# Performance work log

Measured on AMD Instinct MI355X. Metric: run time of the kernel, lower is better.

Reference implementation:

```python
import jax, jax.numpy as jnp
import numpy as np

NUM_HEADS = 16
NUM_KV_HEADS = 4
HEAD_SIZE = 128
SCALE = 1.0 / np.sqrt(128.0).astype(np.float32)
NEG_INF = -1e30


def setup_inputs() -> dict:
    key = jax.random.key(0)
    kq, kk, kv = jax.random.split(key, 3)
    B, S = 2, 2048
    query = jax.random.normal(kq, (B, NUM_HEADS, S, HEAD_SIZE), dtype=jnp.float32)
    k = jax.random.normal(kk, (B, NUM_KV_HEADS, S, HEAD_SIZE), dtype=jnp.float32)
    v = jax.random.normal(kv, (B, NUM_KV_HEADS, S, HEAD_SIZE), dtype=jnp.float32)
    return {"query": query, "key": k, "value": v}


def _attn(query, key, value):
    # query: [B, H, S, D]; key/value: [B, Hkv, S, D]; GQA with group = H // Hkv
    B, H, S, D = query.shape
    Hkv = key.shape[1]
    G = H // Hkv
    q = query.reshape(B, Hkv, G, S, D)
    # scores: [B, Hkv, G, Sq, Sk]
    scores = jnp.einsum('bkgsd,bktd->bkgst', q, key) * jnp.float32(SCALE)
    causal = jnp.tril(jnp.ones((S, S), dtype=bool))  # [Sq, Sk]
    scores = jnp.where(causal, scores, jnp.float32(NEG_INF))
    probs = jax.nn.softmax(scores, axis=-1)
    out = jnp.einsum('bkgst,bktd->bkgsd', probs, value)  # [B, Hkv, G, S, D]
    out = out.reshape(B, H, S, D)
    # transpose(1,2).reshape -> [B, S, H*D]
    return out.transpose(0, 2, 1, 3).reshape(B, S, H * D)


def reference(query, key, value):
    return _attn(query, key, value)
```

## Files before the change

kernel.cpp:

```cpp
#include <hip/hip_runtime.h>


#define S_LEN 2048
#define DH    128
#define NH    16
#define NKVH  4
#define NB    2
#define TQ    128
#define TK    64
#define NQT   (S_LEN / TQ)
#define QSCALE 0.12752749610559243f

typedef __attribute__((ext_vector_type(8))) short short8;
typedef __attribute__((ext_vector_type(4))) float f32x4;

#if __has_builtin(__builtin_amdgcn_exp2f)
#define EX2(x) __builtin_amdgcn_exp2f(x)
#else
#define EX2(x) exp2f(x)
#endif

__device__ __forceinline__ unsigned short bf1(float a) {
    union { float f; unsigned u; } x; x.f = a;
    return (unsigned short)((x.u + 0x8000u) >> 16);
}
__device__ __forceinline__ unsigned pk2(float a, float b) {
    union { float f; unsigned u; } x, y; x.f = a; y.f = b;
    return ((x.u + 0x8000u) >> 16) | ((y.u + 0x8000u) & 0xffff0000u);
}
__device__ __forceinline__ void cp16(const void* g, void* lds) {
    __builtin_amdgcn_global_load_lds(
        (const __attribute__((address_space(1))) void*)g,
        (__attribute__((address_space(3))) void*)lds, 16, 0, 0);
}

__global__ __launch_bounds__(256, 4)
void prepack(const float* __restrict__ K, const float* __restrict__ V,
             unsigned short* __restrict__ Kb, unsigned short* __restrict__ Vt) {
    if (blockIdx.y == 0) {
        const long long flat = (long long)blockIdx.x * 2048 + threadIdx.x * 8;
        const int s = (int)(flat >> 7) & (S_LEN - 1);
        const int d0 = (int)flat & 127;
        const float* p = K + flat;
        float4 x = *(const float4*)p;
        float4 y = *(const float4*)(p + 4);
        const int cs = (d0 >> 3) ^ (s & 7);
        uint4 o;
        o.x = pk2(x.x, x.y); o.y = pk2(x.z, x.w);
        o.z = pk2(y.x, y.y); o.w = pk2(y.z, y.w);
        *(uint4*)(Kb + (flat & ~127LL) + cs * 8) = o;
    } else {
        const int x = blockIdx.x;
        const int bkvh = x >> 7, sblk = (x >> 2) & 31, q = x & 3;
        const int tid = threadIdx.x;
        __shared__ unsigned Lt[64][17];
        const float* base = V + (size_t)bkvh * S_LEN * DH + (size_t)sblk * 64 * DH + q * 32;
#pragma unroll
        for (int j = 0; j < 2; ++j) {
            const int e = tid + j * 256;
            const int s = e >> 3, c4 = e & 7;
            float4 v = *(const float4*)(base + (size_t)s * DH + c4 * 4);
            Lt[s][c4 * 2]     = pk2(v.x, v.y);
            Lt[s][c4 * 2 + 1] = pk2(v.z, v.w);
        }
        __syncthreads();
        const unsigned short* lt = (const unsigned short*)&Lt[0][0];
        const int d_loc = tid >> 3, pc = tid & 7;
        const int d = q * 32 + d_loc;
        const int c_log = pc ^ (d & 7);
        unsigned short vv[8];
#pragma unroll
        for (int j = 0; j < 8; ++j) {
            const int kp = c_log * 8 + j;
            const int kv = (kp & 3) * 16 + (kp >> 2);
            vv[j] = lt[kv * 34 + d_loc];
        }
        uint4 o;
        o.x = (unsigned)vv[0] | ((unsigned)vv[1] << 16);
        o.y = (unsigned)vv[2] | ((unsigned)vv[3] << 16);
        o.z = (unsigned)vv[4] | ((unsigned)vv[5] << 16);
        o.w = (unsigned)vv[6] | ((unsigned)vv[7] << 16);
        *(uint4*)(Vt + (size_t)bkvh * S_LEN * DH + (size_t)d * S_LEN + sblk * 64 + pc * 8) = o;
    }
}

__global__ __launch_bounds__(256, 2)
void attn_fwd(const float* __restrict__ Q,
              const unsigned short* __restrict__ Kb,
              const unsigned short* __restrict__ Vtg,
              float* __restrict__ O) {
    const int n  = blockIdx.x;
    const int x  = n & 15;
    const int h  = (n >> 4) & 15;
    const int b  = n >> 8;
    const int qt = b ? x : (NQT - 1 - x);
    const int kvh = h >> 2;

    const int tid  = threadIdx.x;
    const int w    = tid >> 6;
    const int lane = tid & 63;
    const int quad = lane >> 4;
    const int l16  = lane & 15;
    const int swz  = l16 & 7;

    __shared__ alignas(16) unsigned short Kl[2][TK][DH];
    __shared__ alignas(16) unsigned short Vl[DH][TK];
    __shared__ alignas(16) unsigned short Pl[TQ][TK];

    const unsigned short* kb = Kb  + ((size_t)b * NKVH + kvh) * (size_t)(S_LEN * DH);
    const unsigned short* vb = Vtg + ((size_t)b * NKVH + kvh) * (size_t)(S_LEN * DH);

    const int wq0 = qt * TQ + w * 32;
    short8 aq[2][4];
#pragma unroll
    for (int sub = 0; sub < 2; ++sub) {
        const float* qp = Q + (((size_t)b * NH + h) * S_LEN + wq0 + sub * 16 + l16) * DH;
#pragma unroll
        for (int dc = 0; dc < 4; ++dc) {
            float4 xx = *(const float4*)(qp + dc * 32 + quad * 8);
            float4 yy = *(const float4*)(qp + dc * 32 + quad * 8 + 4);
            union { unsigned u[4]; short8 s; } t;
            t.u[0] = pk2(xx.x * QSCALE, xx.y * QSCALE);
            t.u[1] = pk2(xx.z * QSCALE, xx.w * QSCALE);
            t.u[2] = pk2(yy.x * QSCALE, yy.y * QSCALE);
            t.u[3] = pk2(yy.z * QSCALE, yy.w * QSCALE);
            aq[sub][dc] = t.s;
        }
    }

    f32x4 o[2][8];
#pragma unroll
    for (int sub = 0; sub < 2; ++sub)
#pragma unroll
        for (int ch = 0; ch < 8; ++ch) o[sub][ch] = (f32x4){0.f, 0.f, 0.f, 0.f};
    float lsum[2][4];
#pragma unroll
    for (int sub = 0; sub < 2; ++sub)
#pragma unroll
        for (int r = 0; r < 4; ++r) lsum[sub][r] = 0.f;

    const int nt  = 2 * qt + 2;
    const int ntw = 2 * qt + 1 + (w >> 1);

#pragma unroll
    for (int i = 0; i < 4; ++i)
        cp16((const char*)kb + w * 4096 + i * 1024 + lane * 16,
             (char*)&Kl[0][0][0] + w * 4096 + i * 1024);
    __syncthreads();

    for (int t = 0; t < nt; ++t) {
        const int j0 = t * TK;
#pragma unroll
        for (int i = 0; i < 4; ++i) {
            const int row  = w * 32 + i * 8 + (lane >> 3);
            const int colB = (lane & 7) * 16;
            cp16((const char*)vb + (size_t)row * (S_LEN * 2) + j0 * 2 + colB,
                 (char*)&Vl[0][0] + w * 4096 + i * 1024);
        }
        if (t + 1 < nt) {
            const char* ks = (const char*)(kb + (size_t)(j0 + TK) * DH);
            char* kd = (char*)&Kl[(t + 1) & 1][0][0];
#pragma unroll
            for (int i = 0; i < 4; ++i)
                cp16(ks + w * 4096 + i * 1024 + lane * 16, kd + w * 4096 + i * 1024);
        }

        const unsigned short (*Kc)[DH] = Kl[t & 1];
        const bool active = (t < ntw);
        const bool diag = (t == ntw - 1);
        f32x4 s[2][4];

        if (active) {
#pragma unroll
            for (int sub = 0; sub < 2; ++sub)
#pragma unroll
                for (int k4 = 0; k4 < 4; ++k4) s[sub][k4] = (f32x4){0.f, 0.f, 0.f, 0.f};
#pragma unroll
            for (int dc = 0; dc < 4; ++dc) {
#pragma unroll
                for (int k4 = 0; k4 < 4; ++k4) {
                    short8 bk = *(const short8*)&Kc[k4 * 16 + l16][((dc * 4 + quad) ^ swz) * 8];
                    s[0][k4] = __builtin_amdgcn_mfma_f32_16x16x32_bf16(aq[0][dc], bk, s[0][k4], 0, 0, 0);
                    s[1][k4] = __builtin_amdgcn_mfma_f32_16x16x32_bf16(aq[1][dc], bk, s[1][k4], 0, 0, 0);
                }
            }
#pragma unroll
            for (int sub = 0; sub < 2; ++sub) {
                const int rb = wq0 + sub * 16 + quad * 4;
#pragma unroll
                for (int r = 0; r < 4; ++r) {
                    float v0 = s[sub][0][r], v1 = s[sub][1][r];
                    float v2 = s[sub][2][r], v3 = s[sub][3][r];
                    if (diag) {
                        const int row = rb + r;
                        if (j0 + l16      > row) v0 = -1e30f;
                        if (j0 + 16 + l16 > row) v1 = -1e30f;
                        if (j0 + 32 + l16 > row) v2 = -1e30f;
                        if (j0 + 48 + l16 > row) v3 = -1e30f;
                    }
                    float p0 = EX2(v0), p1 = EX2(v1), p2 = EX2(v2), p3 = EX2(v3);
                    lsum[sub][r] += (p0 + p1) + (p2 + p3);
                    const int prow = w * 32 + sub * 16 + quad * 4 + r;
                    const int chs = (l16 >> 1) ^ (prow & 7);
                    *(uint2*)&Pl[prow][chs * 8 + (l16 & 1) * 4] =
                        make_uint2(pk2(p0, p1), pk2(p2, p3));
                }
            }
        }

        __syncthreads();

        if (active) {
#pragma unroll
            for (int kc = 0; kc < 2; ++kc) {
                const int pr0 = w * 32 + l16;
                short8 ap0 = *(const short8*)&Pl[pr0][(((kc * 4 + quad) ^ swz)) * 8];
                short8 ap1 = *(const short8*)&Pl[pr0 + 16][(((kc * 4 + quad) ^ swz)) * 8];
#pragma unroll
                for (int ch = 0; ch < 8; ++ch) {
                    short8 bv = *(const short8*)&Vl[ch * 16 + l16][((kc * 4 + quad) ^ swz) * 8];
                    o[0][ch] = __builtin_amdgcn_mfma_f32_16x16x32_bf16(ap0, bv, o[0][ch], 0, 0, 0);
                    o[1][ch] = __builtin_amdgcn_mfma_f32_16x16x32_bf16(ap1, bv, o[1][ch], 0, 0, 0);
                }
            }
        }

        __syncthreads();
    }

#pragma unroll
    for (int sub = 0; sub < 2; ++sub) {
#pragma unroll
        for (int r = 0; r < 4; ++r) {
            float rs = lsum[sub][r];
            rs += __shfl_xor(rs, 1);
            rs += __shfl_xor(rs, 2);
            rs += __shfl_xor(rs, 4);
            rs += __shfl_xor(rs, 8);
            const float invl = 1.f / rs;
            const int row = wq0 + sub * 16 + quad * 4 + r;
            float* op = O + ((size_t)b * S_LEN + row) * (NH * DH) + h * DH;
#pragma unroll
            for (int ch = 0; ch < 8; ++ch)
                op[ch * 16 + l16] = o[sub][ch][r] * invl;
        }
    }
}

extern "C" void kernel_launch(void* const* d_in, const int* in_sizes, int n_in,
                              void* d_out, int out_size, void* d_ws, size_t ws_size,
                              hipStream_t stream) {
    const float* Q = (const float*)d_in[0];
    const float* K = (const float*)d_in[1];
    const float* V = (const float*)d_in[2];
    float* O = (float*)d_out;
    unsigned short* Kb = (unsigned short*)d_ws;
    unsigned short* Vt = Kb + (size_t)NB * NKVH * S_LEN * DH;
    dim3 pgrid(NB * NKVH * (S_LEN / 16), 2);
    prepack<<<pgrid, 256, 0, stream>>>(K, V, Kb, Vt);
    attn_fwd<<<dim3(512), 256, 0, stream>>>(Q, Kb, Vt, O);
}
```

Baseline: 158.6 us.

## Split long causal query tiles across blocks and add partial-sum combine kernel

```diff
diff --git a/kernel.cpp b/kernel.cpp
--- a/kernel.cpp
+++ b/kernel.cpp
@@ -10,6 +10,7 @@
 #define TK    64
 #define NQT   (S_LEN / TQ)
 #define QSCALE 0.12752749610559243f
+#define NSPLIT 11
 
 typedef __attribute__((ext_vector_type(8))) short short8;
 typedef __attribute__((ext_vector_type(4))) float f32x4;
@@ -20,9 +21,19 @@
 #define EX2(x) exp2f(x)
 #endif
 
+__constant__ signed char SLOT_QT[16][2] = {
+    {15,-1},{15,-1},{14,-1},{14,-1},{13, 0},{13,-1},{12, 2},{12, 1},
+    {11, 5},{11, 5},{10, 6},{10, 6},{ 9, 7},{ 9, 7},{ 4, 3},{ 8, 8}};
+__constant__ signed char SLOT_MODE[16][2] = {
+    { 0,-1},{ 1,-1},{ 0,-1},{ 1,-1},{ 0, 2},{ 1,-1},{ 0, 2},{ 1, 2},
+    { 0, 0},{ 1, 1},{ 0, 0},{ 1, 1},{ 0, 0},{ 1, 1},{ 2, 2},{ 0, 1}};
+
 __device__ __forceinline__ unsigned short bf1(float a) {
     union { float f; unsigned u; } x; x.f = a;
     return (unsigned short)((x.u + 0x8000u) >> 16);
+}
+__device__ __forceinline__ float bf2f(unsigned short a) {
+    union { float f; unsigned u; } x; x.u = (unsigned)a << 16; return x.f;
 }
 __device__ __forceinline__ unsigned pk2(float a, float b) {
     union { float f; unsigned u; } x, y; x.f = a; y.f = b;
@@ -88,13 +99,18 @@
 void attn_fwd(const float* __restrict__ Q,
               const unsigned short* __restrict__ Kb,
               const unsigned short* __restrict__ Vtg,
-              float* __restrict__ O) {
-    const int n  = blockIdx.x;
-    const int x  = n & 15;
-    const int h  = (n >> 4) & 15;
-    const int b  = n >> 8;
-    const int qt = b ? x : (NQT - 1 - x);
-    const int kvh = h >> 2;
+              float* __restrict__ O,
+              unsigned short* __restrict__ OP,
+              float* __restrict__ LP) {
+    const int n   = blockIdx.x;
+    const int xcd = n & 7;
+    const int b   = xcd >> 2;
+    const int kvh = xcd & 3;
+    const int j   = n >> 3;
+    const int hl  = j >> 4;
+    const int slot = j & 15;
+    const int h   = kvh * 4 + hl;
+    const int hh  = xcd * 4 + hl;
 
     const int tid  = threadIdx.x;
     const int w    = tid >> 6;
@@ -107,143 +123,205 @@
     __shared__ alignas(16) unsigned short Vl[DH][TK];
     __shared__ alignas(16) unsigned short Pl[TQ][TK];
 
-    const unsigned short* kb = Kb  + ((size_t)b * NKVH + kvh) * (size_t)(S_LEN * DH);
-    const unsigned short* vb = Vtg + ((size_t)b * NKVH + kvh) * (size_t)(S_LEN * DH);
-
-    const int wq0 = qt * TQ + w * 32;
-    short8 aq[2][4];
-#pragma unroll
-    for (int sub = 0; sub < 2; ++sub) {
-        const float* qp = Q + (((size_t)b * NH + h) * S_LEN + wq0 + sub * 16 + l16) * DH;
-#pragma unroll
-        for (int dc = 0; dc < 4; ++dc) {
-            float4 xx = *(const float4*)(qp + dc * 32 + quad * 8);
-            float4 yy = *(const float4*)(qp + dc * 32 + quad * 8 + 4);
-            union { unsigned u[4]; short8 s; } t;
-            t.u[0] = pk2(xx.x * QSCALE, xx.y * QSCALE);
-            t.u[1] = pk2(xx.z * QSCALE, xx.w * QSCALE);
-            t.u[2] = pk2(yy.x * QSCALE, yy.y * QSCALE);
-            t.u[3] = pk2(yy.z * QSCALE, yy.w * QSCALE);
-            aq[sub][dc] = t.s;
-        }
-    }
-
-    f32x4 o[2][8];
-#pragma unroll
-    for (int sub = 0; sub < 2; ++sub)
-#pragma unroll
-        for (int ch = 0; ch < 8; ++ch) o[sub][ch] = (f32x4){0.f, 0.f, 0.f, 0.f};
-    float lsum[2][4];
-#pragma unroll
-    for (int sub = 0; sub < 2; ++sub)
-#pragma unroll
-        for (int r = 0; r < 4; ++r) lsum[sub][r] = 0.f;
-
-    const int nt  = 2 * qt + 2;
-    const int ntw = 2 * qt + 1 + (w >> 1);
-
-#pragma unroll
-    for (int i = 0; i < 4; ++i)
-        cp16((const char*)kb + w * 4096 + i * 1024 + lane * 16,
-             (char*)&Kl[0][0][0] + w * 4096 + i * 1024);
-    __syncthreads();
-
-    for (int t = 0; t < nt; ++t) {
-        const int j0 = t * TK;
-#pragma unroll
-        for (int i = 0; i < 4; ++i) {
-            const int row  = w * 32 + i * 8 + (lane >> 3);
-            const int colB = (lane & 7) * 16;
-            cp16((const char*)vb + (size_t)row * (S_LEN * 2) + j0 * 2 + colB,
-                 (char*)&Vl[0][0] + w * 4096 + i * 1024);
-        }
-        if (t + 1 < nt) {
-            const char* ks = (const char*)(kb + (size_t)(j0 + TK) * DH);
-            char* kd = (char*)&Kl[(t + 1) & 1][0][0];
-#pragma unroll
-            for (int i = 0; i < 4; ++i)
-                cp16(ks + w * 4096 + i * 1024 + lane * 16, kd + w * 4096 + i * 1024);
-        }
-
-        const unsigned short (*Kc)[DH] = Kl[t & 1];
-        const bool active = (t < ntw);
-        const bool diag = (t == ntw - 1);
-        f32x4 s[2][4];
-
-        if (active) {
-#pragma unroll
-            for (int sub = 0; sub < 2; ++sub)
-#pragma unroll
-                for (int k4 = 0; k4 < 4; ++k4) s[sub][k4] = (f32x4){0.f, 0.f, 0.f, 0.f};
+    const unsigned short* kb = Kb  + (size_t)xcd * (S_LEN * DH);
+    const unsigned short* vb = Vtg + (size_t)xcd * (S_LEN * DH);
+
+    for (int it = 0; it < 2; ++it) {
+        const int qt   = SLOT_QT[slot][it];
+        const int mode = SLOT_MODE[slot][it];
+        if (mode < 0) continue;
+        const int nt   = 2 * qt + 2;
+        const int t_lo = (mode == 1) ? (qt + 1) : 0;
+        const int t_hi = (mode == 0) ? (qt + 1) : nt;
+        const int Tw   = 2 * qt + 1 + (w >> 1);
+
+        const int wq0 = qt * TQ + w * 32;
+        short8 aq[2][4];
+#pragma unroll
+        for (int sub = 0; sub < 2; ++sub) {
+            const float* qp = Q + (((size_t)b * NH + h) * S_LEN + wq0 + sub * 16 + l16) * DH;
 #pragma unroll
             for (int dc = 0; dc < 4; ++dc) {
-#pragma unroll
-                for (int k4 = 0; k4 < 4; ++k4) {
-                    short8 bk = *(const short8*)&Kc[k4 * 16 + l16][((dc * 4 + quad) ^ swz) * 8];
-                    s[0][k4] = __builtin_amdgcn_mfma_f32_16x16x32_bf16(aq[0][dc], bk, s[0][k4], 0, 0, 0);
-                    s[1][k4] = __builtin_amdgcn_mfma_f32_16x16x32_bf16(aq[1][dc], bk, s[1][k4], 0, 0, 0);
-                }
-            }
+                float4 xx = *(const float4*)(qp + dc * 32 + quad * 8);
+                float4 yy = *(const float4*)(qp + dc * 32 + quad * 8 + 4);
+                union { unsigned u[4]; short8 s; } tt;
+                tt.u[0] = pk2(xx.x * QSCALE, xx.y * QSCALE);
+                tt.u[1] = pk2(xx.z * QSCALE, xx.w * QSCALE);
+                tt.u[2] = pk2(yy.x * QSCALE, yy.y * QSCALE);
+                tt.u[3] = pk2(yy.z * QSCALE, yy.w * QSCALE);
+                aq[sub][dc] = tt.s;
+            }
+        }
+
+        f32x4 o[2][8];
+#pragma unroll
+        for (int sub = 0; sub < 2; ++sub)
+#pragma unroll
+            for (int ch = 0; ch < 8; ++ch) o[sub][ch] = (f32x4){0.f, 0.f, 0.f, 0.f};
+        float lsum[2][4];
+#pragma unroll
+        for (int sub = 0; sub < 2; ++sub)
+#pragma unroll
+            for (int r = 0; r < 4; ++r) lsum[sub][r] = 0.f;
+
+#pragma unroll
+        for (int i = 0; i < 4; ++i)
+            cp16((const char*)(kb + (size_t)t_lo * TK * DH) + w * 4096 + i * 1024 + lane * 16,
+                 (char*)&Kl[t_lo & 1][0][0] + w * 4096 + i * 1024);
+        __syncthreads();
+
+        for (int t = t_lo; t < t_hi; ++t) {
+            const int j0 = t * TK;
+#pragma unroll
+            for (int i = 0; i < 4; ++i) {
+                const int row  = w * 32 + i * 8 + (lane >> 3);
+                const int colB = (lane & 7) * 16;
+                cp16((const char*)vb + (size_t)row * (S_LEN * 2) + j0 * 2 + colB,
+                     (char*)&Vl[0][0] + w * 4096 + i * 1024);
+            }
+            if (t + 1 < t_hi) {
+                const char* ks = (const char*)(kb + (size_t)(j0 + TK) * DH);
+                char* kd = (char*)&Kl[(t + 1) & 1][0][0];
+#pragma unroll
+                for (int i = 0; i < 4; ++i)
+                    cp16(ks + w * 4096 + i * 1024 + lane * 16, kd + w * 4096 + i * 1024);
+            }
+
+            const unsigned short (*Kc)[DH] = Kl[t & 1];
+            const bool active = (t < Tw);
+            const bool diag = (t == Tw - 1);
+            f32x4 s[2][4];
+
+            if (active) {
+#pragma unroll
+                for (int sub = 0; sub < 2; ++sub)
+#pragma unroll
+                    for (int k4 = 0; k4 < 4; ++k4) s[sub][k4] = (f32x4){0.f, 0.f, 0.f, 0.f};
+#pragma unroll
+                for (int dc = 0; dc < 4; ++dc) {
+#pragma unroll
+                    for (int k4 = 0; k4 < 4; ++k4) {
+                        short8 bk = *(const short8*)&Kc[k4 * 16 + l16][((dc * 4 + quad) ^ swz) * 8];
+                        s[0][k4] = __builtin_amdgcn_mfma_f32_16x16x32_bf16(aq[0][dc], bk, s[0][k4], 0, 0, 0);
+                        s[1][k4] = __builtin_amdgcn_mfma_f32_16x16x32_bf16(aq[1][dc], bk, s[1][k4], 0, 0, 0);
+                    }
+                }
+#pragma unroll
+                for (int sub = 0; sub < 2; ++sub) {
+                    const int rb = wq0 + sub * 16 + quad * 4;
+#pragma unroll
+                    for (int r = 0; r < 4; ++r) {
+                        float v0 = s[sub][0][r], v1 = s[sub][1][r];
+                        float v2 = s[sub][2][r], v3 = s[sub][3][r];
+                        if (diag) {
+                            const int row = rb + r;
+                            if (j0 + l16      > row) v0 = -1e30f;
+                            if (j0 + 16 + l16 > row) v1 = -1e30f;
+                            if (j0 + 32 + l16 > row) v2 = -1e30f;
+                            if (j0 + 48 + l16 > row) v3 = -1e30f;
+                        }
+                        float p0 = EX2(v0), p1 = EX2(v1), p2 = EX2(v2), p3 = EX2(v3);
+                        lsum[sub][r] += (p0 + p1) + (p2 + p3);
+                        const int prow = w * 32 + sub * 16 + quad * 4 + r;
+                        const int chs = (l16 >> 1) ^ (prow & 7);
+                        *(uint2*)&Pl[prow][chs * 8 + (l16 & 1) * 4] =
+                            make_uint2(pk2(p0, p1), pk2(p2, p3));
+                    }
+                }
+            }
+
+            __syncthreads();
+
+            if (active) {
+#pragma unroll
+                for (int kc = 0; kc < 2; ++kc) {
+                    const int pr0 = w * 32 + l16;
+                    short8 ap0 = *(const short8*)&Pl[pr0][(((kc * 4 + quad) ^ swz)) * 8];
+                    short8 ap1 = *(const short8*)&Pl[pr0 + 16][(((kc * 4 + quad) ^ swz)) * 8];
+#pragma unroll
+                    for (int ch = 0; ch < 8; ++ch) {
+                        short8 bv = *(const short8*)&Vl[ch * 16 + l16][((kc * 4 + quad) ^ swz) * 8];
+                        o[0][ch] = __builtin_amdgcn_mfma_f32_16x16x32_bf16(ap0, bv, o[0][ch], 0, 0, 0);
+                        o[1][ch] = __builtin_amdgcn_mfma_f32_16x16x32_bf16(ap1, bv, o[1][ch], 0, 0, 0);
+                    }
+                }
+            }
+
+            __syncthreads();
+        }
+
+        if (mode == 2) {
 #pragma unroll
             for (int sub = 0; sub < 2; ++sub) {
-                const int rb = wq0 + sub * 16 + quad * 4;
 #pragma unroll
                 for (int r = 0; r < 4; ++r) {
-                    float v0 = s[sub][0][r], v1 = s[sub][1][r];
-                    float v2 = s[sub][2][r], v3 = s[sub][3][r];
-                    if (diag) {
-                        const int row = rb + r;
-                        if (j0 + l16      > row) v0 = -1e30f;
-                        if (j0 + 16 + l16 > row) v1 = -1e30f;
-                        if (j0 + 32 + l16 > row) v2 = -1e30f;
-                        if (j0 + 48 + l16 > row) v3 = -1e30f;
-                    }
-                    float p0 = EX2(v0), p1 = EX2(v1), p2 = EX2(v2), p3 = EX2(v3);
-                    lsum[sub][r] += (p0 + p1) + (p2 + p3);
-                    const int prow = w * 32 + sub * 16 + quad * 4 + r;
-                    const int chs = (l16 >> 1) ^ (prow & 7);
-                    *(uint2*)&Pl[prow][chs * 8 + (l16 & 1) * 4] =
-                        make_uint2(pk2(p0, p1), pk2(p2, p3));
-                }
-            }
-        }
-
-        __syncthreads();
-
-        if (active) {
-#pragma unroll
-            for (int kc = 0; kc < 2; ++kc) {
-                const int pr0 = w * 32 + l16;
-                short8 ap0 = *(const short8*)&Pl[pr0][(((kc * 4 + quad) ^ swz)) * 8];
-                short8 ap1 = *(const short8*)&Pl[pr0 + 16][(((kc * 4 + quad) ^ swz)) * 8];
-#pragma unroll
-                for (int ch = 0; ch < 8; ++ch) {
-                    short8 bv = *(const short8*)&Vl[ch * 16 + l16][((kc * 4 + quad) ^ swz) * 8];
-                    o[0][ch] = __builtin_amdgcn_mfma_f32_16x16x32_bf16(ap0, bv, o[0][ch], 0, 0, 0);
-                    o[1][ch] = __builtin_amdgcn_mfma_f32_16x16x32_bf16(ap1, bv, o[1][ch], 0, 0, 0);
-                }
-            }
-        }
-
+                    float rs = lsum[sub][r];
+                    rs += __shfl_xor(rs, 1);
+                    rs += __shfl_xor(rs, 2);
+                    rs += __shfl_xor(rs, 4);
+                    rs += __shfl_xor(rs, 8);
+                    const float invl = 1.f / rs;
+                    const int row = wq0 + sub * 16 + quad * 4 + r;
+                    float* op = O + ((size_t)b * S_LEN + row) * (NH * DH) + h * DH;
+#pragma unroll
+                    for (int ch = 0; ch < 8; ++ch)
+                        op[ch * 16 + l16] = o[sub][ch][r] * invl;
+                }
+            }
+        } else {
+            const size_t pbase = ((size_t)(hh * NSPLIT + (qt - 5)) * 2 + mode) * (128 * 128);
+            unsigned short* opp = OP + pbase;
+            float* lpp = LP + ((size_t)(hh * NSPLIT + (qt - 5)) * 2 + mode) * 128;
+#pragma unroll
+            for (int sub = 0; sub < 2; ++sub) {
+#pragma unroll
+                for (int r = 0; r < 4; ++r) {
+                    float rs = lsum[sub][r];
+                    rs += __shfl_xor(rs, 1);
+                    rs += __shfl_xor(rs, 2);
+                    rs += __shfl_xor(rs, 4);
+                    rs += __shfl_xor(rs, 8);
+                    const int lrow = w * 32 + sub * 16 + quad * 4 + r;
+                    if (l16 == 0) lpp[lrow] = rs;
+#pragma unroll
+                    for (int ch = 0; ch < 8; ++ch)
+                        opp[(size_t)lrow * 128 + ch * 16 + l16] = bf1(o[sub][ch][r]);
+                }
+            }
+        }
         __syncthreads();
     }
-
-#pragma unroll
-    for (int sub = 0; sub < 2; ++sub) {
-#pragma unroll
-        for (int r = 0; r < 4; ++r) {
-            float rs = lsum[sub][r];
-            rs += __shfl_xor(rs, 1);
-            rs += __shfl_xor(rs, 2);
-            rs += __shfl_xor(rs, 4);
-            rs += __shfl_xor(rs, 8);
-            const float invl = 1.f / rs;
-            const int row = wq0 + sub * 16 + quad * 4 + r;
-            float* op = O + ((size_t)b * S_LEN + row) * (NH * DH) + h * DH;
-#pragma unroll
-            for (int ch = 0; ch < 8; ++ch)
-                op[ch * 16 + l16] = o[sub][ch][r] * invl;
-        }
+}
+
+__global__ __launch_bounds__(256, 4)
+void combine(const unsigned short* __restrict__ OP, const float* __restrict__ LP,
+             float* __restrict__ O) {
+    const int cb = blockIdx.x;
+    const int hh = cb / NSPLIT, qi = cb - hh * NSPLIT;
+    const int qt = qi + 5;
+    const int b = hh >> 4, kvh = (hh >> 2) & 3, hl = hh & 3, h = kvh * 4 + hl;
+    __shared__ float Linv[128];
+    if (threadIdx.x < 128) {
+        const size_t lb = (size_t)(hh * NSPLIT + qi) * 2 * 128;
+        Linv[threadIdx.x] = 1.f / (LP[lb + threadIdx.x] + LP[lb + 128 + threadIdx.x]);
+    }
+    __syncthreads();
+    const unsigned short* pa = OP + (size_t)(hh * NSPLIT + qi) * 2 * 16384;
+    const unsigned short* pb = pa + 16384;
+    float* ob = O + ((size_t)b * S_LEN + qt * 128) * (NH * DH) + h * DH;
+#pragma unroll
+    for (int i = 0; i < 16; ++i) {
+        const int flat = i * 1024 + threadIdx.x * 4;
+        const int row = flat >> 7, d = flat & 127;
+        ushort4 a = *(const ushort4*)(pa + flat);
+        ushort4 bq = *(const ushort4*)(pb + flat);
+        const float inv = Linv[row];
+        float4 r;
+        r.x = (bf2f(a.x) + bf2f(bq.x)) * inv;
+        r.y = (bf2f(a.y) + bf2f(bq.y)) * inv;
+        r.z = (bf2f(a.z) + bf2f(bq.z)) * inv;
+        r.w = (bf2f(a.w) + bf2f(bq.w)) * inv;
+        *(float4*)(ob + (size_t)row * (NH * DH) + d) = r;
     }
 }
 
@@ -256,7 +334,10 @@
     float* O = (float*)d_out;
     unsigned short* Kb = (unsigned short*)d_ws;
     unsigned short* Vt = Kb + (size_t)NB * NKVH * S_LEN * DH;
+    unsigned short* OP = Vt + (size_t)NB * NKVH * S_LEN * DH;
+    float* LP = (float*)(OP + (size_t)32 * NSPLIT * 2 * 128 * 128);
     dim3 pgrid(NB * NKVH * (S_LEN / 16), 2);
     prepack<<<pgrid, 256, 0, stream>>>(K, V, Kb, Vt);
-    attn_fwd<<<dim3(512), 256, 0, stream>>>(Q, Kb, Vt, O);
-}
+    attn_fwd<<<dim3(512), 256, 0, stream>>>(Q, Kb, Vt, O, OP, LP);
+    combine<<<dim3(32 * NSPLIT), 256, 0, stream>>>(OP, LP, O);
+}
```

Result: faster. 154.8 us (-2.3%).
